# Performance work log

Hardware: AMD Instinct MI355X
Metric: run time of the kernel (lower is better)

## Reference

```python
import jax, jax.numpy as jnp
import numpy as np

B, L, DIN, DM, NL = 2, 1024, 512, 1024, 4
E, N, R, K = 2048, 16, 64, 4  # d_inner, d_state, dt_rank, d_conv


def setup_inputs() -> dict:
    key = jax.random.key(0)
    ks = iter(jax.random.split(key, 32))
    rn = lambda sh, s=1.0: jax.random.normal(next(ks), sh, jnp.float32) * s
    A_init = jnp.broadcast_to(jnp.arange(1, N + 1, dtype=jnp.float32), (NL, E, N))
    return dict(
        x=rn((B, L, DIN)),
        z=rn((B, L, DIN)),
        ip_w=rn((DM, DIN), 0.02), ip_b=jnp.zeros((DM,), jnp.float32),
        ln_w=jnp.ones((NL, DM), jnp.float32), ln_b=jnp.zeros((NL, DM), jnp.float32),
        inproj_w=rn((NL, 2 * E, DM), 0.02),
        conv_w=rn((NL, E, K), 0.1), conv_b=jnp.zeros((NL, E), jnp.float32),
        xproj_w=rn((NL, R + 2 * N, E), 0.02),
        dtproj_w=rn((NL, E, R), 0.05), dtproj_b=rn((NL, E), 0.1),
        A_log=jnp.log(A_init),
        Dp=jnp.ones((NL, E), jnp.float32),
        outproj_w=rn((NL, DM, E), 0.02),
        fnorm_w=jnp.ones((DM,), jnp.float32), fnorm_b=jnp.zeros((DM,), jnp.float32),
        op_w=rn((DIN, DM), 0.02), op_b=jnp.zeros((DIN,), jnp.float32),
    )


def layernorm(x, w, b, eps=1e-5):
    m = x.mean(-1, keepdims=True)
    v = ((x - m) ** 2).mean(-1, keepdims=True)
    return (x - m) * jax.lax.rsqrt(v + eps) * w + b


def dwconv_causal(xm, w, b):
    # xm: (B, L, E); w: (E, K) depthwise kernel; causal left padding
    xc = xm.transpose(0, 2, 1)  # (B, E, L)
    out = jax.lax.conv_general_dilated(
        xc, w[:, None, :], (1,), [(K - 1, 0)],
        feature_group_count=E, dimension_numbers=('NCH', 'OIH', 'NCH'))
    return (out + b[:, None]).transpose(0, 2, 1)


def selective_scan(u, dt, A, Bm, Cm, D):
    # u, dt: (B, L, E); A: (E, N); Bm, Cm: (B, L, N); D: (E,)
    h0 = jnp.zeros((u.shape[0], E, N), u.dtype)

    def step(h, inp):
        dt_t, u_t, B_t, C_t = inp  # (B,E),(B,E),(B,N),(B,N)
        dA = jnp.exp(dt_t[..., None] * A)                      # (B, E, N)
        h = dA * h + (dt_t * u_t)[..., None] * B_t[:, None, :]  # (B, E, N)
        y = jnp.einsum('ben,bn->be', h, C_t)
        return h, y

    _, ys = jax.lax.scan(step, h0, (dt.transpose(1, 0, 2), u.transpose(1, 0, 2),
                                    Bm.transpose(1, 0, 2), Cm.transpose(1, 0, 2)))
    return ys.transpose(1, 0, 2) + u * D  # (B, L, E)


def mamba_block(x, inproj_w, conv_w, conv_b, xproj_w, dtproj_w, dtproj_b, A_log, Dp, outproj_w):
    xz = jnp.einsum('bld,ed->ble', x, inproj_w)  # (B, L, 2E)
    xm, zg = xz[..., :E], xz[..., E:]
    xm = jax.nn.silu(dwconv_causal(xm, conv_w, conv_b))
    x_dbl = jnp.einsum('ble,re->blr', xm, xproj_w)  # (B, L, R+2N)
    dt = jax.nn.softplus(jnp.einsum('blr,er->ble', x_dbl[..., :R], dtproj_w) + dtproj_b)
    Bm = x_dbl[..., R:R + N]
    Cm = x_dbl[..., R + N:]
    A = -jnp.exp(A_log)  # (E, N)
    y = selective_scan(xm, dt, A, Bm, Cm, Dp)
    y = y * jax.nn.silu(zg)
    return jnp.einsum('ble,de->bld', y, outproj_w)


def reference(x, z, ip_w, ip_b, ln_w, ln_b, inproj_w, conv_w, conv_b, xproj_w,
              dtproj_w, dtproj_b, A_log, Dp, outproj_w, fnorm_w, fnorm_b, op_w, op_b):
    # z is accepted but unused, matching the original forward(x, z)
    h = jnp.einsum('bld,hd->blh', x, ip_w) + ip_b
    for l in range(NL):
        hn = layernorm(h, ln_w[l], ln_b[l])
        h = h + mamba_block(hn, inproj_w[l], conv_w[l], conv_b[l], xproj_w[l],
                            dtproj_w[l], dtproj_b[l], A_log[l], Dp[l], outproj_w[l])
    h = layernorm(h, fnorm_w, fnorm_b)
    return jnp.einsum('blh,oh->blo', h, op_w) + op_b
```

## Files before the change

### kernel.cpp

```cpp
#include <hip/hip_runtime.h>
#include <math.h>

#define BB 2
#define LL 1024
#define DIN_ 512
#define DM_ 1024
#define NL_ 4
#define EE 2048
#define NN 16
#define RR 64
#define KK 4

#define NC 32
#define CT 32

typedef unsigned short ushort_t;
typedef unsigned int uint_t;

using frag_ab = __attribute__((ext_vector_type(8))) short;
using frag_cd = __attribute__((ext_vector_type(4))) float;

__device__ __forceinline__ float softplus_f(float x) {
    return fmaxf(x, 0.f) + log1pf(expf(-fabsf(x)));
}
__device__ __forceinline__ float silu_fast(float x) {
    return x / (1.f + __expf(-x));
}
__device__ __forceinline__ float bf2f(ushort_t x) {
    return __uint_as_float((uint_t)x << 16);
}
__device__ __forceinline__ ushort_t f2bf(float x) {
    uint_t u = __float_as_uint(x);
    uint_t r = (u + 0x7fffu + ((u >> 16) & 1u)) >> 16;
    return (ushort_t)r;
}
__device__ __forceinline__ uint_t f2bf2(float lo, float hi) {
    return (uint_t)f2bf(lo) | ((uint_t)f2bf(hi) << 16);
}
__device__ __forceinline__ void gload_lds16(const void* g, void* l) {
    __builtin_amdgcn_global_load_lds(
        (const __attribute__((address_space(1))) void*)g,
        (__attribute__((address_space(3))) void*)l, 16, 0, 0);
}

struct CvtArgs {
    const float* src[6];
    ushort_t* dst[6];
    int cum[7];
};

__global__ __launch_bounds__(256) void cvt_all_kernel(CvtArgs a)
{
    const int total = a.cum[6];
    const int stride = gridDim.x * 256;
    for (int i = blockIdx.x * 256 + threadIdx.x; i < total; i += stride) {
        int s = 0;
#pragma unroll
        for (int k = 1; k < 6; k++) s += (i >= a.cum[k]) ? 1 : 0;
        int j = i - a.cum[s];
        const float4* src = (const float4*)a.src[s];
        float4 v0 = src[2 * j];
        float4 v1 = src[2 * j + 1];
        uint4 u;
        u.x = f2bf2(v0.x, v0.y);
        u.y = f2bf2(v0.z, v0.w);
        u.z = f2bf2(v1.x, v1.y);
        u.w = f2bf2(v1.z, v1.w);
        ((uint4*)a.dst[s])[j] = u;
    }
}

template <int EPI, int NT, int OUTBF>
__global__ __launch_bounds__(256) void mgemm_kernel(
    void* __restrict__ Cp, const ushort_t* __restrict__ A,
    const ushort_t* __restrict__ W, const float* __restrict__ bias,
    int N, int K, int lda, int ldw, int ldc, int pstride)
{
    __shared__ __attribute__((aligned(16))) ushort_t smem[2][(8 + NT) * 1024];

    const int tid = threadIdx.x;
    const int w = tid >> 6;
    const int lane = tid & 63;
    const int r = lane & 15;
    const int q = lane >> 4;
    const int m0 = blockIdx.y * 128;
    const int n0 = blockIdx.x * (NT * 16);
    const int wm = w >> 1;
    const int wn = w & 1;
    const int NWT = NT / 2;

    frag_cd acc[4][NWT];
#pragma unroll
    for (int i = 0; i < 4; i++)
#pragma unroll
        for (int j = 0; j < NWT; j++)
#pragma unroll
            for (int t = 0; t < 4; t++) acc[i][j][t] = 0.f;

    size_t koff = (EPI == 5) ? (size_t)blockIdx.z * K : 0;
    const ushort_t* Ab = A + (size_t)m0 * lda + koff;
    const ushort_t* Wb = W + (size_t)n0 * ldw + koff;

    constexpr int FPW = (8 + NT) * 2 / 4;
    const ushort_t* gp[FPW];
    bool ok[FPW];
#pragma unroll
    for (int fi = 0; fi < FPW; fi++) {
        int F = w + fi * 4;
        int kk = F & 1;
        int G = F >> 1;
        if (G < 8) {
            gp[fi] = Ab + (size_t)(G * 16 + r) * lda + kk * 32 + q * 8;
            ok[fi] = true;
        } else {
            int nt = G - 8;
            ok[fi] = (n0 + nt * 16 + r) < N;
            gp[fi] = Wb + (size_t)(nt * 16 + r) * ldw + kk * 32 + q * 8;
        }
    }

    auto stage = [&](int buf) {
#pragma unroll
        for (int fi = 0; fi < FPW; fi++) {
            if (ok[fi])
                gload_lds16(gp[fi], &smem[buf][(w + fi * 4) * 512]);
            gp[fi] += 64;
        }
    };

    stage(0);
    int buf = 0;
    for (int k0 = 0; k0 < K; k0 += 64) {
        __syncthreads();
        if (k0 + 64 < K) stage(buf ^ 1);
#pragma unroll
        for (int kk = 0; kk < 2; kk++) {
            frag_ab af[4], bf[NWT];
#pragma unroll
            for (int i = 0; i < 4; i++)
                af[i] = *(const frag_ab*)(&smem[buf][((wm * 4 + i) * 2 + kk) * 512] + lane * 8);
#pragma unroll
            for (int j = 0; j < NWT; j++)
                bf[j] = *(const frag_ab*)(&smem[buf][((8 + wn * NWT + j) * 2 + kk) * 512] + lane * 8);
#pragma unroll
            for (int i = 0; i < 4; i++)
#pragma unroll
                for (int j = 0; j < NWT; j++)
                    acc[i][j] = __builtin_amdgcn_mfma_f32_16x16x32_bf16(
                        af[i], bf[j], acc[i][j], 0, 0, 0);
        }
        buf ^= 1;
    }

    float* Cf = (float*)Cp;
    ushort_t* Cb = (ushort_t*)Cp;
    float* Cpart = (EPI == 5) ? Cf + (size_t)blockIdx.z * pstride : Cf;
#pragma unroll
    for (int i = 0; i < 4; i++) {
        int mrow = m0 + (wm * 4 + i) * 16 + q * 4;
#pragma unroll
        for (int j = 0; j < NWT; j++) {
            int col = n0 + (wn * NWT + j) * 16 + r;
            if (col >= N) continue;
            float bv = (EPI == 2) ? bias[col] : 0.f;
#pragma unroll
            for (int t = 0; t < 4; t++) {
                float v = acc[i][j][t];
                size_t idx = (size_t)(mrow + t) * ldc + col;
                if (EPI == 5) { Cpart[idx] = v; continue; }
                if (EPI == 2) v = softplus_f(v + bv);
                if (OUTBF) Cb[idx] = f2bf(v);
                else       Cf[idx] = v;
            }
        }
    }
}

__global__ __launch_bounds__(256) void dt_kernel(
    float* __restrict__ dtb, const float* __restrict__ xdb,
    const float* __restrict__ W, const float* __restrict__ bias)
{
    const int tid = threadIdx.x;
    const int e = blockIdx.x * 256 + tid;
    const int t0 = blockIdx.y * 16;

    __shared__ float xs[16][64];
    {
        int tt = tid >> 4;
        int k4 = tid & 15;
        float4 v = *(const float4*)(xdb + (size_t)(t0 + tt) * 96 + k4 * 4);
        *(float4*)&xs[tt][k4 * 4] = v;
    }

    float4 wr[16];
    const float4* Wr = (const float4*)(W + (size_t)e * RR);
#pragma unroll
    for (int i = 0; i < 16; i++) wr[i] = Wr[i];
    const float bv = bias[e];
    __syncthreads();

#pragma unroll 4
    for (int t = 0; t < 16; t++) {
        float a0 = 0.f, a1 = 0.f, a2 = 0.f, a3 = 0.f;
#pragma unroll
        for (int k4 = 0; k4 < 16; k4++) {
            float4 xk = *(const float4*)&xs[t][k4 * 4];
            float4 wk = wr[k4];
            a0 = fmaf(wk.x, xk.x, a0);
            a1 = fmaf(wk.y, xk.y, a1);
            a2 = fmaf(wk.z, xk.z, a2);
            a3 = fmaf(wk.w, xk.w, a3);
        }
        dtb[(size_t)(t0 + t) * EE + e] = softplus_f((a0 + a1) + (a2 + a3) + bv);
    }
}

__global__ __launch_bounds__(256) void reduce_ln_kernel(
    float* __restrict__ h, ushort_t* __restrict__ hn,
    const float* __restrict__ parts, int nparts, int pstride4,
    const float* __restrict__ bias,
    const float* __restrict__ w, const float* __restrict__ b, int hasres)
{
    const int row = blockIdx.x;
    const int tid = threadIdx.x;
    const int i4 = row * (DM_ / 4) + tid;

    float4 v = make_float4(0.f, 0.f, 0.f, 0.f);
    if (hasres) v = ((const float4*)h)[i4];
    for (int p = 0; p < nparts; p++) {
        float4 t = ((const float4*)parts)[(size_t)p * pstride4 + i4];
        v.x += t.x; v.y += t.y; v.z += t.z; v.w += t.w;
    }
    if (bias) {
        float4 t = ((const float4*)bias)[tid];
        v.x += t.x; v.y += t.y; v.z += t.z; v.w += t.w;
    }
    ((float4*)h)[i4] = v;

    float s = v.x + v.y + v.z + v.w;
    float sq = v.x * v.x + v.y * v.y + v.z * v.z + v.w * v.w;
#pragma unroll
    for (int off = 32; off; off >>= 1) {
        s += __shfl_down(s, off);
        sq += __shfl_down(sq, off);
    }
    __shared__ float ls[4], lq[4];
    int wid = tid >> 6;
    if ((tid & 63) == 0) { ls[wid] = s; lq[wid] = sq; }
    __syncthreads();
    float S = ls[0] + ls[1] + ls[2] + ls[3];
    float Q = lq[0] + lq[1] + lq[2] + lq[3];
    float mean = S * (1.f / DM_);
    float var = Q * (1.f / DM_) - mean * mean;
    float inv = rsqrtf(var + 1e-5f);
    float4 wv = ((const float4*)w)[tid];
    float4 bv = ((const float4*)b)[tid];
    ushort4 o;
    o.x = f2bf((v.x - mean) * inv * wv.x + bv.x);
    o.y = f2bf((v.y - mean) * inv * wv.y + bv.y);
    o.z = f2bf((v.z - mean) * inv * wv.z + bv.z);
    o.w = f2bf((v.w - mean) * inv * wv.w + bv.w);
    ((ushort4*)hn)[i4] = o;
}

__global__ __launch_bounds__(256) void reduce_xdb_kernel(
    float* __restrict__ xdb,
    const float* __restrict__ parts, int pstride4, int total4)
{
    int i = blockIdx.x * 256 + threadIdx.x;
    if (i >= total4) return;
    float4 v = make_float4(0.f, 0.f, 0.f, 0.f);
#pragma unroll
    for (int p = 0; p < 16; p++) {
        float4 t = ((const float4*)parts)[(size_t)p * pstride4 + i];
        v.x += t.x; v.y += t.y; v.z += t.z; v.w += t.w;
    }
    ((float4*)xdb)[i] = v;
}

__global__ __launch_bounds__(256) void reduce_bias_kernel(
    float* __restrict__ out, const float* __restrict__ parts,
    const float* __restrict__ bias, int pstride4, int n4, int total4)
{
    int i = blockIdx.x * 256 + threadIdx.x;
    if (i >= total4) return;
    float4 v = ((const float4*)bias)[i % n4];
#pragma unroll
    for (int p = 0; p < 4; p++) {
        float4 t = ((const float4*)parts)[(size_t)p * pstride4 + i];
        v.x += t.x; v.y += t.y; v.z += t.z; v.w += t.w;
    }
    ((float4*)out)[i] = v;
}

__global__ __launch_bounds__(256) void conv_silu_kernel(
    ushort_t* __restrict__ xm, const ushort_t* __restrict__ xz,
    const float* __restrict__ cw, const float* __restrict__ cb)
{
    const int e = blockIdx.x * 256 + threadIdx.x;
    const int t0 = blockIdx.y * 4;
    const int b = blockIdx.z;
    const ushort_t* X = xz + (size_t)b * LL * 2 * EE + e;
    float4 w4 = ((const float4*)cw)[e];
    float wk[4] = {w4.x, w4.y, w4.z, w4.w};
    float cbv = cb[e];
    float v[7];
#pragma unroll
    for (int k = 0; k < 7; k++) {
        int t = t0 - 3 + k;
        v[k] = (t >= 0) ? bf2f(X[(size_t)t * 2 * EE]) : 0.f;
    }
    ushort_t* Y = xm + ((size_t)b * LL + t0) * EE + e;
#pragma unroll
    for (int j = 0; j < 4; j++) {
        float acc = cbv;
#pragma unroll
        for (int k = 0; k < 4; k++) acc = fmaf(wk[k], v[j + k], acc);
        Y[(size_t)j * EE] = f2bf(silu_fast(acc));
    }
}

__global__ __launch_bounds__(256) void scan_phase1_kernel(
    float* __restrict__ Pg, float* __restrict__ Sg,
    const float* __restrict__ dt, const ushort_t* __restrict__ u,
    const float* __restrict__ xdb, const float* __restrict__ A_log)
{
    const int tid = threadIdx.x;
    const int e = blockIdx.x * 256 + tid;
    const int c = blockIdx.y;
    const int b = blockIdx.z;
    const int t0 = c * CT;

    __shared__ float Bs[CT][16];
    {
        int tt = tid >> 3;
        int jj = tid & 7;
        if (jj < 4) {
            float4 v = *(const float4*)(xdb + ((size_t)(b * LL + t0 + tt) * 96 + 64 + jj * 4));
            *(float4*)&Bs[tt][jj * 4] = v;
        }
    }
    __syncthreads();

    float Ae[16];
#pragma unroll
    for (int k = 0; k < 4; k++) {
        float4 a = *(const float4*)(A_log + (size_t)e * NN + k * 4);
        Ae[k * 4 + 0] = -__expf(a.x);
        Ae[k * 4 + 1] = -__expf(a.y);
        Ae[k * 4 + 2] = -__expf(a.z);
        Ae[k * 4 + 3] = -__expf(a.w);
    }

    float S[16];
#pragma unroll
    for (int n = 0; n < 16; n++) S[n] = 0.f;
    float Dsum = 0.f;

    const float* dt_p = dt + (size_t)(b * LL + t0) * EE + e;
    const ushort_t* u_p = u + (size_t)(b * LL + t0) * EE + e;

    float dtv = dt_p[0];
    float uv = bf2f(u_p[0]);
#pragma unroll 4
    for (int i = 0; i < CT; i++) {
        int ip = (i + 1 < CT) ? i + 1 : i;
        float dtn = dt_p[(size_t)ip * EE];
        float un = bf2f(u_p[(size_t)ip * EE]);
        float dtu = dtv * uv;
        Dsum += dtv;
        float Bv[16];
#pragma unroll
        for (int k = 0; k < 4; k++)
            *(float4*)&Bv[k * 4] = *(const float4*)&Bs[i][k * 4];
#pragma unroll
        for (int n = 0; n < 16; n++) {
            float da = __expf(dtv * Ae[n]);
            S[n] = fmaf(da, S[n], dtu * Bv[n]);
        }
        dtv = dtn; uv = un;
    }

    size_t o = ((size_t)(b * NC + c) * EE + e) * 16;
#pragma unroll
    for (int k = 0; k < 4; k++) {
        float4 p4;
        p4.x = __expf(Dsum * Ae[k * 4 + 0]);
        p4.y = __expf(Dsum * Ae[k * 4 + 1]);
        p4.z = __expf(Dsum * Ae[k * 4 + 2]);
        p4.w = __expf(Dsum * Ae[k * 4 + 3]);
        *(float4*)(Pg + o + k * 4) = p4;
        *(float4*)(Sg + o + k * 4) = *(float4*)&S[k * 4];
    }
}

__global__ __launch_bounds__(256) void scan_combine_kernel(
    float* __restrict__ Pg, const float* __restrict__ Sg)
{
    const int f = blockIdx.x * 256 + threadIdx.x;
    const int b = blockIdx.y;
    const size_t stride = (size_t)EE * 16;
    const size_t base = (size_t)b * NC * stride + f;

    float P[NC], S[NC];
#pragma unroll
    for (int c = 0; c < NC; c++) {
        P[c] = Pg[base + c * stride];
        S[c] = Sg[base + c * stride];
    }
    float h = 0.f;
#pragma unroll
    for (int c = 0; c < NC; c++) {
        h = fmaf(P[c], h, S[c]);
        P[c] = h;
    }
#pragma unroll
    for (int c = 0; c < NC; c++)
        Pg[base + c * stride] = P[c];
}

__global__ __launch_bounds__(256) void scan_phase2_kernel(
    ushort_t* __restrict__ y, const float* __restrict__ Pg,
    const float* __restrict__ dt, const ushort_t* __restrict__ u,
    const float* __restrict__ xdb, const ushort_t* __restrict__ xz,
    const float* __restrict__ A_log, const float* __restrict__ Dp)
{
    const int tid = threadIdx.x;
    const int e = blockIdx.x * 256 + tid;
    const int c = blockIdx.y;
    const int b = blockIdx.z;
    const int t0 = c * CT;

    __shared__ float Bs[CT][16], Cs[CT][16];
    {
        int tt = tid >> 3;
        int jj = tid & 7;
        float4 v = *(const float4*)(xdb + ((size_t)(b * LL + t0 + tt) * 96 + 64 + jj * 4));
        if (jj < 4) *(float4*)&Bs[tt][jj * 4] = v;
        else        *(float4*)&Cs[tt][(jj - 4) * 4] = v;
    }
    __syncthreads();

    float Ae[16];
#pragma unroll
    for (int k = 0; k < 4; k++) {
        float4 a = *(const float4*)(A_log + (size_t)e * NN + k * 4);
        Ae[k * 4 + 0] = -__expf(a.x);
        Ae[k * 4 + 1] = -__expf(a.y);
        Ae[k * 4 + 2] = -__expf(a.z);
        Ae[k * 4 + 3] = -__expf(a.w);
    }

    float h[16];
    if (c == 0) {
#pragma unroll
        for (int n = 0; n < 16; n++) h[n] = 0.f;
    } else {
        size_t o = ((size_t)(b * NC + (c - 1)) * EE + e) * 16;
#pragma unroll
        for (int k = 0; k < 4; k++)
            *(float4*)&h[k * 4] = *(const float4*)(Pg + o + k * 4);
    }

    const float Dv = Dp[e];
    const float* dt_p = dt + (size_t)(b * LL + t0) * EE + e;
    const ushort_t* u_p = u + (size_t)(b * LL + t0) * EE + e;
    const ushort_t* zg_p = xz + (size_t)(b * LL + t0) * 2 * EE + EE + e;
    ushort_t* y_p = y + (size_t)(b * LL + t0) * EE + e;

    float dtv = dt_p[0];
    float uv = bf2f(u_p[0]);
    float zv = bf2f(zg_p[0]);
#pragma unroll 4
    for (int i = 0; i < CT; i++) {
        int ip = (i + 1 < CT) ? i + 1 : i;
        float dtn = dt_p[(size_t)ip * EE];
        float un = bf2f(u_p[(size_t)ip * EE]);
        float zn = bf2f(zg_p[(size_t)ip * 2 * EE]);
        float dtu = dtv * uv;
        float Bv[16], Cv[16];
#pragma unroll
        for (int k = 0; k < 4; k++) {
            *(float4*)&Bv[k * 4] = *(const float4*)&Bs[i][k * 4];
            *(float4*)&Cv[k * 4] = *(const float4*)&Cs[i][k * 4];
        }
        float yv = 0.f;
#pragma unroll
        for (int n = 0; n < 16; n++) {
            float da = __expf(dtv * Ae[n]);
            h[n] = fmaf(da, h[n], dtu * Bv[n]);
            yv = fmaf(h[n], Cv[n], yv);
        }
        y_p[(size_t)i * EE] = f2bf((yv + uv * Dv) * silu_fast(zv));
        dtv = dtn; uv = un; zv = zn;
    }
}

extern "C" void kernel_launch(void* const* d_in, const int* in_sizes, int n_in,
                              void* d_out, int out_size, void* d_ws, size_t ws_size,
                              hipStream_t stream)
{
    const float* x = (const float*)d_in[0];
    const float* ip_w = (const float*)d_in[2];
    const float* ip_b = (const float*)d_in[3];
    const float* ln_w = (const float*)d_in[4];
    const float* ln_b = (const float*)d_in[5];
    const float* inproj_w = (const float*)d_in[6];
    const float* conv_w = (const float*)d_in[7];
    const float* conv_b = (const float*)d_in[8];
    const float* xproj_w = (const float*)d_in[9];
    const float* dtproj_w = (const float*)d_in[10];
    const float* dtproj_b = (const float*)d_in[11];
    const float* A_log = (const float*)d_in[12];
    const float* Dp = (const float*)d_in[13];
    const float* outproj_w = (const float*)d_in[14];
    const float* fnorm_w = (const float*)d_in[15];
    const float* fnorm_b = (const float*)d_in[16];
    const float* op_w = (const float*)d_in[17];
    const float* op_b = (const float*)d_in[18];
    float* out = (float*)d_out;

    const size_t BL = (size_t)BB * LL;

    float* fp = (float*)d_ws;
    float* h = fp;           fp += BL * DM_;
    float* xdb = fp;         fp += BL * 96;
    float* dtb = fp;         fp += BL * EE;
    float* Pg = fp;          fp += (size_t)BB * NC * EE * 16;
    float* Sg = fp;          fp += (size_t)BB * NC * EE * 16;
    float* parts = dtb;
    ushort_t* us = (ushort_t*)fp;
    ushort_t* xb = us;       us += BL * DIN_;
    ushort_t* hnb = us;      us += BL * DM_;
    ushort_t* xzb = us;      us += BL * 2 * EE;
    ushort_t* xm = us;       us += BL * EE;
    ushort_t* yb = us;       us += BL * EE;
    ushort_t* ipwb = us;     us += (size_t)DM_ * DIN_;
    ushort_t* inprojb = us;  us += (size_t)NL_ * 2 * EE * DM_;
    ushort_t* xprojb = us;   us += (size_t)NL_ * 96 * EE;
    ushort_t* outprojb = us; us += (size_t)NL_ * DM_ * EE;
    ushort_t* opwb = us;     us += (size_t)DIN_ * DM_;

    dim3 blk(256);

    {
        CvtArgs a;
        const float* srcs[6] = {x, ip_w, inproj_w, xproj_w, outproj_w, op_w};
        ushort_t* dsts[6] = {xb, ipwb, inprojb, xprojb, outprojb, opwb};
        size_t ns[6] = {BL * DIN_, (size_t)DM_ * DIN_, (size_t)NL_ * 2 * EE * DM_,
                        (size_t)NL_ * 96 * EE,
                        (size_t)NL_ * DM_ * EE, (size_t)DIN_ * DM_};
        int cum = 0;
        for (int s = 0; s < 6; s++) {
            a.src[s] = srcs[s];
            a.dst[s] = dsts[s];
            a.cum[s] = cum;
            cum += (int)(ns[s] / 8);
        }
        a.cum[6] = cum;
        int nblk = (cum + 255) / 256;
        if (nblk > 2048) nblk = 2048;
        cvt_all_kernel<<<dim3(nblk), blk, 0, stream>>>(a);
    }

    const int PS_DM = (int)(BL * DM_);

    mgemm_kernel<5, 4, 0><<<dim3(DM_ / 64, BL / 128, 2), blk, 0, stream>>>(
        parts, xb, ipwb, nullptr, DM_, DIN_ / 2, DIN_, DIN_, DM_, PS_DM);
    reduce_ln_kernel<<<dim3(BL), blk, 0, stream>>>(
        h, hnb, parts, 2, PS_DM / 4, ip_b, ln_w, ln_b, 0);

    for (int l = 0; l < NL_; l++) {
        mgemm_kernel<0, 8, 1><<<dim3(2 * EE / 128, BL / 128), blk, 0, stream>>>(
            xzb, hnb, inprojb + (size_t)l * 2 * EE * DM_, nullptr,
            2 * EE, DM_, DM_, DM_, 2 * EE, 0);
        conv_silu_kernel<<<dim3(EE / 256, LL / 4, BB), blk, 0, stream>>>(
            xm, xzb, conv_w + l * EE * KK, conv_b + l * EE);
        mgemm_kernel<5, 8, 0><<<dim3(1, BL / 128, 16), blk, 0, stream>>>(
            parts, xm, xprojb + (size_t)l * 96 * EE, nullptr,
            96, EE / 16, EE, EE, 96, (int)(BL * 96));
        reduce_xdb_kernel<<<dim3((int)(BL * 96 / 4 + 255) / 256), blk, 0, stream>>>(
            xdb, parts, (int)(BL * 96 / 4), (int)(BL * 96 / 4));
        dt_kernel<<<dim3(EE / 256, BL / 16), blk, 0, stream>>>(
            dtb, xdb, dtproj_w + (size_t)l * EE * RR, dtproj_b + (size_t)l * EE);

        scan_phase1_kernel<<<dim3(EE / 256, NC, BB), blk, 0, stream>>>(
            Pg, Sg, dtb, xm, xdb, A_log + (size_t)l * EE * NN);
        scan_combine_kernel<<<dim3(EE * 16 / 256, BB), blk, 0, stream>>>(Pg, Sg);
        scan_phase2_kernel<<<dim3(EE / 256, NC, BB), blk, 0, stream>>>(
            yb, Pg, dtb, xm, xdb, xzb, A_log + (size_t)l * EE * NN, Dp + l * EE);

        mgemm_kernel<5, 8, 0><<<dim3(DM_ / 128, BL / 128, 4), blk, 0, stream>>>(
            parts, yb, outprojb + (size_t)l * DM_ * EE, nullptr,
            DM_, EE / 4, EE, EE, DM_, PS_DM);
        const float* nw = (l + 1 < NL_) ? ln_w + (l + 1) * DM_ : fnorm_w;
        const float* nb = (l + 1 < NL_) ? ln_b + (l + 1) * DM_ : fnorm_b;
        reduce_ln_kernel<<<dim3(BL), blk, 0, stream>>>(
            h, hnb, parts, 4, PS_DM / 4, nullptr, nw, nb, 1);
    }

    mgemm_kernel<5, 4, 0><<<dim3(DIN_ / 64, BL / 128, 4), blk, 0, stream>>>(
        parts, hnb, opwb, nullptr, DIN_, DM_ / 4, DM_, DM_, DIN_, (int)(BL * DIN_));
    reduce_bias_kernel<<<dim3((int)(BL * DIN_ / 4 + 255) / 256), blk, 0, stream>>>(
        out, parts, op_b, (int)(BL * DIN_ / 4), DIN_ / 4, (int)(BL * DIN_ / 4));
}
```

Before: 922.5 us.

## Fuse dt projection and softplus into both selective-scan phases

Removes the separate dt_kernel and the fp32 dt buffer. Each scan phase now recomputes dt per timestep from the x_dbl row, with the 64-wide dt projection weights held in registers. This avoids writing and twice re-reading a BL×E fp32 tensor and drops one launch per layer. The cost is that the 64-FMA dot product is computed twice, once in each phase, and the extra weight registers may lower occupancy. The conversion kernel also drops its grid-stride loop in favour of one element per thread with an uncapped grid.

```diff
diff --git a/kernel.cpp b/kernel.cpp
--- a/kernel.cpp
+++ b/kernel.cpp
@@ -51,23 +51,21 @@
 
 __global__ __launch_bounds__(256) void cvt_all_kernel(CvtArgs a)
 {
-    const int total = a.cum[6];
-    const int stride = gridDim.x * 256;
-    for (int i = blockIdx.x * 256 + threadIdx.x; i < total; i += stride) {
-        int s = 0;
-#pragma unroll
-        for (int k = 1; k < 6; k++) s += (i >= a.cum[k]) ? 1 : 0;
-        int j = i - a.cum[s];
-        const float4* src = (const float4*)a.src[s];
-        float4 v0 = src[2 * j];
-        float4 v1 = src[2 * j + 1];
-        uint4 u;
-        u.x = f2bf2(v0.x, v0.y);
-        u.y = f2bf2(v0.z, v0.w);
-        u.z = f2bf2(v1.x, v1.y);
-        u.w = f2bf2(v1.z, v1.w);
-        ((uint4*)a.dst[s])[j] = u;
-    }
+    int i = blockIdx.x * 256 + threadIdx.x;
+    if (i >= a.cum[6]) return;
+    int s = 0;
+#pragma unroll
+    for (int k = 1; k < 6; k++) s += (i >= a.cum[k]) ? 1 : 0;
+    int j = i - a.cum[s];
+    const float4* src = (const float4*)a.src[s];
+    float4 v0 = src[2 * j];
+    float4 v1 = src[2 * j + 1];
+    uint4 u;
+    u.x = f2bf2(v0.x, v0.y);
+    u.y = f2bf2(v0.z, v0.w);
+    u.z = f2bf2(v1.x, v1.y);
+    u.w = f2bf2(v1.z, v1.w);
+    ((uint4*)a.dst[s])[j] = u;
 }
 
 template <int EPI, int NT, int OUTBF>
@@ -162,56 +160,15 @@
         for (int j = 0; j < NWT; j++) {
             int col = n0 + (wn * NWT + j) * 16 + r;
             if (col >= N) continue;
-            float bv = (EPI == 2) ? bias[col] : 0.f;
 #pragma unroll
             for (int t = 0; t < 4; t++) {
                 float v = acc[i][j][t];
                 size_t idx = (size_t)(mrow + t) * ldc + col;
                 if (EPI == 5) { Cpart[idx] = v; continue; }
-                if (EPI == 2) v = softplus_f(v + bv);
                 if (OUTBF) Cb[idx] = f2bf(v);
                 else       Cf[idx] = v;
             }
         }
-    }
-}
-
-__global__ __launch_bounds__(256) void dt_kernel(
-    float* __restrict__ dtb, const float* __restrict__ xdb,
-    const float* __restrict__ W, const float* __restrict__ bias)
-{
-    const int tid = threadIdx.x;
-    const int e = blockIdx.x * 256 + tid;
-    const int t0 = blockIdx.y * 16;
-
-    __shared__ float xs[16][64];
-    {
-        int tt = tid >> 4;
-        int k4 = tid & 15;
-        float4 v = *(const float4*)(xdb + (size_t)(t0 + tt) * 96 + k4 * 4);
-        *(float4*)&xs[tt][k4 * 4] = v;
-    }
-
-    float4 wr[16];
-    const float4* Wr = (const float4*)(W + (size_t)e * RR);
-#pragma unroll
-    for (int i = 0; i < 16; i++) wr[i] = Wr[i];
-    const float bv = bias[e];
-    __syncthreads();
-
-#pragma unroll 4
-    for (int t = 0; t < 16; t++) {
-        float a0 = 0.f, a1 = 0.f, a2 = 0.f, a3 = 0.f;
-#pragma unroll
-        for (int k4 = 0; k4 < 16; k4++) {
-            float4 xk = *(const float4*)&xs[t][k4 * 4];
-            float4 wk = wr[k4];
-            a0 = fmaf(wk.x, xk.x, a0);
-            a1 = fmaf(wk.y, xk.y, a1);
-            a2 = fmaf(wk.z, xk.z, a2);
-            a3 = fmaf(wk.w, xk.w, a3);
-        }
-        dtb[(size_t)(t0 + t) * EE + e] = softplus_f((a0 + a1) + (a2 + a3) + bv);
     }
 }
 
@@ -320,10 +277,27 @@
     }
 }
 
+__device__ __forceinline__ float dt_inline(
+    const float* __restrict__ xr, const float4* __restrict__ wr, float dbias)
+{
+    float a0 = 0.f, a1 = 0.f, a2 = 0.f, a3 = 0.f;
+#pragma unroll
+    for (int k4 = 0; k4 < 16; k4++) {
+        float4 xk = *(const float4*)(xr + k4 * 4);
+        float4 wk = wr[k4];
+        a0 = fmaf(wk.x, xk.x, a0);
+        a1 = fmaf(wk.y, xk.y, a1);
+        a2 = fmaf(wk.z, xk.z, a2);
+        a3 = fmaf(wk.w, xk.w, a3);
+    }
+    return softplus_f((a0 + a1) + (a2 + a3) + dbias);
+}
+
 __global__ __launch_bounds__(256) void scan_phase1_kernel(
     float* __restrict__ Pg, float* __restrict__ Sg,
-    const float* __restrict__ dt, const ushort_t* __restrict__ u,
-    const float* __restrict__ xdb, const float* __restrict__ A_log)
+    const ushort_t* __restrict__ u, const float* __restrict__ xdb,
+    const float* __restrict__ A_log,
+    const float* __restrict__ dtW, const float* __restrict__ dtB)
 {
     const int tid = threadIdx.x;
     const int e = blockIdx.x * 256 + tid;
@@ -340,7 +314,12 @@
             *(float4*)&Bs[tt][jj * 4] = v;
         }
     }
-    __syncthreads();
+
+    float4 wr[16];
+    const float4* Wr = (const float4*)(dtW + (size_t)e * RR);
+#pragma unroll
+    for (int i = 0; i < 16; i++) wr[i] = Wr[i];
+    const float dbias = dtB[e];
 
     float Ae[16];
 #pragma unroll
@@ -351,22 +330,20 @@
         Ae[k * 4 + 2] = -__expf(a.z);
         Ae[k * 4 + 3] = -__expf(a.w);
     }
+    __syncthreads();
 
     float S[16];
 #pragma unroll
     for (int n = 0; n < 16; n++) S[n] = 0.f;
     float Dsum = 0.f;
 
-    const float* dt_p = dt + (size_t)(b * LL + t0) * EE + e;
     const ushort_t* u_p = u + (size_t)(b * LL + t0) * EE + e;
-
-    float dtv = dt_p[0];
-    float uv = bf2f(u_p[0]);
+    const float* xrow = xdb + (size_t)(b * LL + t0) * 96;
+
 #pragma unroll 4
     for (int i = 0; i < CT; i++) {
-        int ip = (i + 1 < CT) ? i + 1 : i;
-        float dtn = dt_p[(size_t)ip * EE];
-        float un = bf2f(u_p[(size_t)ip * EE]);
+        float dtv = dt_inline(xrow + (size_t)i * 96, wr, dbias);
+        float uv = bf2f(u_p[(size_t)i * EE]);
         float dtu = dtv * uv;
         Dsum += dtv;
         float Bv[16];
@@ -378,7 +355,6 @@
             float da = __expf(dtv * Ae[n]);
             S[n] = fmaf(da, S[n], dtu * Bv[n]);
         }
-        dtv = dtn; uv = un;
     }
 
     size_t o = ((size_t)(b * NC + c) * EE + e) * 16;
@@ -421,9 +397,10 @@
 
 __global__ __launch_bounds__(256) void scan_phase2_kernel(
     ushort_t* __restrict__ y, const float* __restrict__ Pg,
-    const float* __restrict__ dt, const ushort_t* __restrict__ u,
-    const float* __restrict__ xdb, const ushort_t* __restrict__ xz,
-    const float* __restrict__ A_log, const float* __restrict__ Dp)
+    const ushort_t* __restrict__ u, const float* __restrict__ xdb,
+    const ushort_t* __restrict__ xz,
+    const float* __restrict__ A_log, const float* __restrict__ Dp,
+    const float* __restrict__ dtW, const float* __restrict__ dtB)
 {
     const int tid = threadIdx.x;
     const int e = blockIdx.x * 256 + tid;
@@ -439,7 +416,12 @@
         if (jj < 4) *(float4*)&Bs[tt][jj * 4] = v;
         else        *(float4*)&Cs[tt][(jj - 4) * 4] = v;
     }
-    __syncthreads();
+
+    float4 wr[16];
+    const float4* Wr = (const float4*)(dtW + (size_t)e * RR);
+#pragma unroll
+    for (int i = 0; i < 16; i++) wr[i] = Wr[i];
+    const float dbias = dtB[e];
 
     float Ae[16];
 #pragma unroll
@@ -450,6 +432,7 @@
         Ae[k * 4 + 2] = -__expf(a.z);
         Ae[k * 4 + 3] = -__expf(a.w);
     }
+    __syncthreads();
 
     float h[16];
     if (c == 0) {
@@ -463,20 +446,16 @@
     }
 
     const float Dv = Dp[e];
-    const float* dt_p = dt + (size_t)(b * LL + t0) * EE + e;
     const ushort_t* u_p = u + (size_t)(b * LL + t0) * EE + e;
     const ushort_t* zg_p = xz + (size_t)(b * LL + t0) * 2 * EE + EE + e;
     ushort_t* y_p = y + (size_t)(b * LL + t0) * EE + e;
-
-    float dtv = dt_p[0];
-    float uv = bf2f(u_p[0]);
-    float zv = bf2f(zg_p[0]);
+    const float* xrow = xdb + (size_t)(b * LL + t0) * 96;
+
 #pragma unroll 4
     for (int i = 0; i < CT; i++) {
-        int ip = (i + 1 < CT) ? i + 1 : i;
-        float dtn = dt_p[(size_t)ip * EE];
-        float un = bf2f(u_p[(size_t)ip * EE]);
-        float zn = bf2f(zg_p[(size_t)ip * 2 * EE]);
+        float dtv = dt_inline(xrow + (size_t)i * 96, wr, dbias);
+        float uv = bf2f(u_p[(size_t)i * EE]);
+        float zv = bf2f(zg_p[(size_t)i * 2 * EE]);
         float dtu = dtv * uv;
         float Bv[16], Cv[16];
 #pragma unroll
@@ -492,7 +471,6 @@
             yv = fmaf(h[n], Cv[n], yv);
         }
         y_p[(size_t)i * EE] = f2bf((yv + uv * Dv) * silu_fast(zv));
-        dtv = dtn; uv = un; zv = zn;
     }
 }
 
@@ -525,10 +503,9 @@
     float* fp = (float*)d_ws;
     float* h = fp;           fp += BL * DM_;
     float* xdb = fp;         fp += BL * 96;
-    float* dtb = fp;         fp += BL * EE;
+    float* parts = fp;       fp += BL * EE;
     float* Pg = fp;          fp += (size_t)BB * NC * EE * 16;
     float* Sg = fp;          fp += (size_t)BB * NC * EE * 16;
-    float* parts = dtb;
     ushort_t* us = (ushort_t*)fp;
     ushort_t* xb = us;       us += BL * DIN_;
     ushort_t* hnb = us;      us += BL * DM_;
@@ -558,9 +535,7 @@
             cum += (int)(ns[s] / 8);
         }
         a.cum[6] = cum;
-        int nblk = (cum + 255) / 256;
-        if (nblk > 2048) nblk = 2048;
-        cvt_all_kernel<<<dim3(nblk), blk, 0, stream>>>(a);
+        cvt_all_kernel<<<dim3((cum + 255) / 256), blk, 0, stream>>>(a);
     }
 
     const int PS_DM = (int)(BL * DM_);
@@ -581,14 +556,14 @@
             96, EE / 16, EE, EE, 96, (int)(BL * 96));
         reduce_xdb_kernel<<<dim3((int)(BL * 96 / 4 + 255) / 256), blk, 0, stream>>>(
             xdb, parts, (int)(BL * 96 / 4), (int)(BL * 96 / 4));
-        dt_kernel<<<dim3(EE / 256, BL / 16), blk, 0, stream>>>(
-            dtb, xdb, dtproj_w + (size_t)l * EE * RR, dtproj_b + (size_t)l * EE);
 
         scan_phase1_kernel<<<dim3(EE / 256, NC, BB), blk, 0, stream>>>(
-            Pg, Sg, dtb, xm, xdb, A_log + (size_t)l * EE * NN);
+            Pg, Sg, xm, xdb, A_log + (size_t)l * EE * NN,
+            dtproj_w + (size_t)l * EE * RR, dtproj_b + (size_t)l * EE);
         scan_combine_kernel<<<dim3(EE * 16 / 256, BB), blk, 0, stream>>>(Pg, Sg);
         scan_phase2_kernel<<<dim3(EE / 256, NC, BB), blk, 0, stream>>>(
-            yb, Pg, dtb, xm, xdb, xzb, A_log + (size_t)l * EE * NN, Dp + l * EE);
+            yb, Pg, xm, xdb, xzb, A_log + (size_t)l * EE * NN, Dp + l * EE,
+            dtproj_w + (size_t)l * EE * RR, dtproj_b + (size_t)l * EE);
 
         mgemm_kernel<5, 8, 0><<<dim3(DM_ / 128, BL / 128, 4), blk, 0, stream>>>(
             parts, yb, outprojb + (size_t)l * DM_ * EE, nullptr,
```

Measured after the change: 1.110 ms. 1.2x slower.

## Retile dt projection to two channels per thread; flatten cvt grid

Applied to the files above, without the earlier changes.

The dt projection kernel now has each thread compute two channels over 8 timesteps instead of one channel over 16. Each xs value read from shared memory therefore feeds twice the FMAs, and the grid gets more blocks along time. The weight-conversion kernel drops its grid-stride loop and launches one thread per element with no block cap, trading loop overhead for a much larger grid. Dead bias and softplus epilogue code is also removed from the GEMM template. Holding two weight rows per thread doubles register use in dt_kernel, which may lower occupancy.

```diff
diff --git a/kernel.cpp b/kernel.cpp
--- a/kernel.cpp
+++ b/kernel.cpp
@@ -51,23 +51,21 @@
 
 __global__ __launch_bounds__(256) void cvt_all_kernel(CvtArgs a)
 {
-    const int total = a.cum[6];
-    const int stride = gridDim.x * 256;
-    for (int i = blockIdx.x * 256 + threadIdx.x; i < total; i += stride) {
-        int s = 0;
-#pragma unroll
-        for (int k = 1; k < 6; k++) s += (i >= a.cum[k]) ? 1 : 0;
-        int j = i - a.cum[s];
-        const float4* src = (const float4*)a.src[s];
-        float4 v0 = src[2 * j];
-        float4 v1 = src[2 * j + 1];
-        uint4 u;
-        u.x = f2bf2(v0.x, v0.y);
-        u.y = f2bf2(v0.z, v0.w);
-        u.z = f2bf2(v1.x, v1.y);
-        u.w = f2bf2(v1.z, v1.w);
-        ((uint4*)a.dst[s])[j] = u;
-    }
+    int i = blockIdx.x * 256 + threadIdx.x;
+    if (i >= a.cum[6]) return;
+    int s = 0;
+#pragma unroll
+    for (int k = 1; k < 6; k++) s += (i >= a.cum[k]) ? 1 : 0;
+    int j = i - a.cum[s];
+    const float4* src = (const float4*)a.src[s];
+    float4 v0 = src[2 * j];
+    float4 v1 = src[2 * j + 1];
+    uint4 u;
+    u.x = f2bf2(v0.x, v0.y);
+    u.y = f2bf2(v0.z, v0.w);
+    u.z = f2bf2(v1.x, v1.y);
+    u.w = f2bf2(v1.z, v1.w);
+    ((uint4*)a.dst[s])[j] = u;
 }
 
 template <int EPI, int NT, int OUTBF>
@@ -162,13 +160,11 @@
         for (int j = 0; j < NWT; j++) {
             int col = n0 + (wn * NWT + j) * 16 + r;
             if (col >= N) continue;
-            float bv = (EPI == 2) ? bias[col] : 0.f;
 #pragma unroll
             for (int t = 0; t < 4; t++) {
                 float v = acc[i][j][t];
                 size_t idx = (size_t)(mrow + t) * ldc + col;
                 if (EPI == 5) { Cpart[idx] = v; continue; }
-                if (EPI == 2) v = softplus_f(v + bv);
                 if (OUTBF) Cb[idx] = f2bf(v);
                 else       Cf[idx] = v;
             }
@@ -181,37 +177,48 @@
     const float* __restrict__ W, const float* __restrict__ bias)
 {
     const int tid = threadIdx.x;
-    const int e = blockIdx.x * 256 + tid;
-    const int t0 = blockIdx.y * 16;
-
-    __shared__ float xs[16][64];
-    {
+    const int e0 = blockIdx.x * 512 + tid;
+    const int e1 = e0 + 256;
+    const int t0 = blockIdx.y * 8;
+
+    __shared__ float xs[8][64];
+    if (tid < 128) {
         int tt = tid >> 4;
         int k4 = tid & 15;
         float4 v = *(const float4*)(xdb + (size_t)(t0 + tt) * 96 + k4 * 4);
         *(float4*)&xs[tt][k4 * 4] = v;
     }
 
-    float4 wr[16];
-    const float4* Wr = (const float4*)(W + (size_t)e * RR);
-#pragma unroll
-    for (int i = 0; i < 16; i++) wr[i] = Wr[i];
-    const float bv = bias[e];
+    float4 wa[16], wb[16];
+    const float4* Wa = (const float4*)(W + (size_t)e0 * RR);
+    const float4* Wb = (const float4*)(W + (size_t)e1 * RR);
+#pragma unroll
+    for (int i = 0; i < 16; i++) { wa[i] = Wa[i]; wb[i] = Wb[i]; }
+    const float ba = bias[e0];
+    const float bb = bias[e1];
     __syncthreads();
 
-#pragma unroll 4
-    for (int t = 0; t < 16; t++) {
+#pragma unroll 2
+    for (int t = 0; t < 8; t++) {
         float a0 = 0.f, a1 = 0.f, a2 = 0.f, a3 = 0.f;
+        float c0 = 0.f, c1 = 0.f, c2 = 0.f, c3 = 0.f;
 #pragma unroll
         for (int k4 = 0; k4 < 16; k4++) {
             float4 xk = *(const float4*)&xs[t][k4 * 4];
-            float4 wk = wr[k4];
-            a0 = fmaf(wk.x, xk.x, a0);
-            a1 = fmaf(wk.y, xk.y, a1);
-            a2 = fmaf(wk.z, xk.z, a2);
-            a3 = fmaf(wk.w, xk.w, a3);
-        }
-        dtb[(size_t)(t0 + t) * EE + e] = softplus_f((a0 + a1) + (a2 + a3) + bv);
+            float4 u = wa[k4];
+            float4 v = wb[k4];
+            a0 = fmaf(u.x, xk.x, a0);
+            a1 = fmaf(u.y, xk.y, a1);
+            a2 = fmaf(u.z, xk.z, a2);
+            a3 = fmaf(u.w, xk.w, a3);
+            c0 = fmaf(v.x, xk.x, c0);
+            c1 = fmaf(v.y, xk.y, c1);
+            c2 = fmaf(v.z, xk.z, c2);
+            c3 = fmaf(v.w, xk.w, c3);
+        }
+        float* drow = dtb + (size_t)(t0 + t) * EE;
+        drow[e0] = softplus_f((a0 + a1) + (a2 + a3) + ba);
+        drow[e1] = softplus_f((c0 + c1) + (c2 + c3) + bb);
     }
 }
 
@@ -558,9 +565,7 @@
             cum += (int)(ns[s] / 8);
         }
         a.cum[6] = cum;
-        int nblk = (cum + 255) / 256;
-        if (nblk > 2048) nblk = 2048;
-        cvt_all_kernel<<<dim3(nblk), blk, 0, stream>>>(a);
+        cvt_all_kernel<<<dim3((cum + 255) / 256), blk, 0, stream>>>(a);
     }
 
     const int PS_DM = (int)(BL * DM_);
@@ -581,7 +586,7 @@
             96, EE / 16, EE, EE, 96, (int)(BL * 96));
         reduce_xdb_kernel<<<dim3((int)(BL * 96 / 4 + 255) / 256), blk, 0, stream>>>(
             xdb, parts, (int)(BL * 96 / 4), (int)(BL * 96 / 4));
-        dt_kernel<<<dim3(EE / 256, BL / 16), blk, 0, stream>>>(
+        dt_kernel<<<dim3(EE / 512, BL / 8), blk, 0, stream>>>(
             dtb, xdb, dtproj_w + (size_t)l * EE * RR, dtproj_b + (size_t)l * EE);
 
         scan_phase1_kernel<<<dim3(EE / 256, NC, BB), blk, 0, stream>>>(
```

New measurement: 920.6 us. About the same (-0.2%).
